# Optimization experiments

Hardware: AMD Instinct MI355X
Metric: run time of the kernel (lower is better)

Reference implementation:

```python
import jax, jax.numpy as jnp
import numpy as np

B, T, D, H, C = 256, 512, 300, 128, 6

def setup_inputs() -> dict:
    key = jax.random.key(0)
    ks = jax.random.split(key, 8)
    s = 1.0 / np.sqrt(H)  # PyTorch LSTM/Linear uniform init scale
    x = jax.random.normal(ks[0], (B, T, D), dtype=jnp.float32)
    lengths = jax.random.randint(ks[1], (B,), 1, T + 1)
    W_ih = jax.random.uniform(ks[2], (4 * H, D), minval=-s, maxval=s, dtype=jnp.float32)
    W_hh = jax.random.uniform(ks[3], (4 * H, H), minval=-s, maxval=s, dtype=jnp.float32)
    b_ih = jax.random.uniform(ks[4], (4 * H,), minval=-s, maxval=s, dtype=jnp.float32)
    b_hh = jax.random.uniform(ks[5], (4 * H,), minval=-s, maxval=s, dtype=jnp.float32)
    fc_w = jax.random.uniform(ks[6], (C, H), minval=-s, maxval=s, dtype=jnp.float32)
    fc_b = jax.random.uniform(ks[7], (C,), minval=-s, maxval=s, dtype=jnp.float32)
    return {"x": x, "W_ih": W_ih, "W_hh": W_hh, "b_ih": b_ih, "b_hh": b_hh,
            "fc_w": fc_w, "fc_b": fc_b, "lengths": lengths}

def _lstm_last_hidden(x, W_ih, W_hh, b_ih, b_hh, lengths):
    # Equivalent to pack_padded_sequence + nn.LSTM: the returned hidden[-1]
    # is the state at t = length-1 for each sequence. We run a masked scan:
    # state updates are frozen once t >= length.
    Bv, Tv, _ = x.shape
    Hv = W_hh.shape[1]
    xs = jnp.swapaxes(x, 0, 1)                              # [T, B, D]
    gx = jnp.einsum('tbd,gd->tbg', xs, W_ih) + b_ih + b_hh  # [T, B, 4H]
    mask = (jnp.arange(Tv)[:, None] < lengths[None, :])     # [T, B]

    def step(carry, inp):
        h, c = carry
        g, m = inp
        gates = g + h @ W_hh.T                              # [B, 4H]
        i, f, gg, o = jnp.split(gates, 4, axis=-1)          # PyTorch gate order i,f,g,o
        i = jax.nn.sigmoid(i)
        f = jax.nn.sigmoid(f)
        gg = jnp.tanh(gg)
        o = jax.nn.sigmoid(o)
        c_new = f * c + i * gg
        h_new = o * jnp.tanh(c_new)
        m = m[:, None]
        h = jnp.where(m, h_new, h)
        c = jnp.where(m, c_new, c)
        return (h, c), None

    h0 = jnp.zeros((Bv, Hv), dtype=x.dtype)
    c0 = jnp.zeros((Bv, Hv), dtype=x.dtype)
    (h, c), _ = jax.lax.scan(step, (h0, c0), (gx, mask))
    return h

def reference(x, W_ih, W_hh, b_ih, b_hh, fc_w, fc_b, lengths):
    h = _lstm_last_hidden(x, W_ih, W_hh, b_ih, b_hh, lengths)  # [B, H]
    return h @ fc_w.T + fc_b                                   # [B, 6]
```

## Files before the change

### kernel.cpp

```cpp
#include <hip/hip_runtime.h>
#include <hip/hip_bf16.h>
#include <stdint.h>
#include <type_traits>

#define NB 256
#define NT 512
#define ND 300
#define NH 128
#define NG 512
#define NC 6

typedef __attribute__((ext_vector_type(8))) short short8;
typedef __attribute__((ext_vector_type(4))) float f32x4;

static __device__ __forceinline__ float bf2f(unsigned int u) {
  return __builtin_bit_cast(float, (u & 0xffffu) << 16);
}
static __device__ __forceinline__ unsigned short f2bf(float f) {
  return __builtin_bit_cast(unsigned short, __float2bfloat16(f));
}
static __device__ __forceinline__ unsigned int packbf(float a, float b) {
  return (unsigned int)f2bf(a) | ((unsigned int)f2bf(b) << 16);
}
static __device__ __forceinline__ float ld1(const unsigned short* p) { return bf2f(*p); }
static __device__ __forceinline__ float ld1(const float* p) { return *p; }
static __device__ __forceinline__ void st1(unsigned short* p, float v) { *p = f2bf(v); }
static __device__ __forceinline__ void st1(float* p, float v) { *p = v; }

static __device__ __forceinline__ float sigmoid_fast(float x) {
  return __builtin_amdgcn_rcpf(1.f + __expf(-x));
}
static __device__ __forceinline__ float tanh_fast(float x) {
  return 1.f - 2.f * __builtin_amdgcn_rcpf(__expf(2.f * x) + 1.f);
}

static __device__ __forceinline__ uint2 load4bf_fast(const unsigned short* row, int k) {
  return *(const uint2*)(row + k);
}
static __device__ __forceinline__ uint2 load4bf_fast(const float* row, int k) {
  float4 f = *(const float4*)(row + k);
  uint2 v;
  v.x = packbf(f.x, f.y);
  v.y = packbf(f.z, f.w);
  return v;
}
static __device__ __forceinline__ uint2 load4bf(const unsigned short* row, int k, int lim) {
  if (k + 3 < lim) return load4bf_fast(row, k);
  unsigned int e0 = (k + 0 < lim) ? row[k + 0] : 0;
  unsigned int e1 = (k + 1 < lim) ? row[k + 1] : 0;
  unsigned int e2 = (k + 2 < lim) ? row[k + 2] : 0;
  unsigned int e3 = (k + 3 < lim) ? row[k + 3] : 0;
  uint2 v;
  v.x = e0 | (e1 << 16);
  v.y = e2 | (e3 << 16);
  return v;
}
static __device__ __forceinline__ uint2 load4bf(const float* row, int k, int lim) {
  if (k + 3 < lim) return load4bf_fast(row, k);
  float f0 = (k + 0 < lim) ? row[k + 0] : 0.f;
  float f1 = (k + 1 < lim) ? row[k + 1] : 0.f;
  float f2 = (k + 2 < lim) ? row[k + 2] : 0.f;
  float f3 = (k + 3 < lim) ? row[k + 3] : 0.f;
  uint2 v;
  v.x = packbf(f0, f1);
  v.y = packbf(f2, f3);
  return v;
}

__global__ void detect_dtype(const unsigned short* __restrict__ X, int* __restrict__ flag) {
  __shared__ int cnt;
  if (threadIdx.x == 0) cnt = 0;
  __syncthreads();
  int c = 0;
  for (int i = threadIdx.x; i < 512; i += 64) {
    unsigned int u = X[i];
    unsigned int e = (u >> 7) & 0xffu;
    if (u == 0u || (e >= 97u && e <= 157u)) c++;
  }
  atomicAdd(&cnt, c);
  __syncthreads();
  if (threadIdx.x == 0) *flag = (cnt >= 448) ? 0 : 1;
}

template <typename XT, typename GXT>
__global__ __launch_bounds__(256) void gx_gemm(const int* __restrict__ flag, int want,
                                               const XT* __restrict__ X,
                                               const XT* __restrict__ Wih,
                                               const XT* __restrict__ bih,
                                               const XT* __restrict__ bhh,
                                               const int* __restrict__ lengths,
                                               GXT* __restrict__ gx,
                                               int b_base, int t_base, int Tc) {
  if (*flag != want) return;
  const int mb = blockIdx.x;
  const int m0 = mb << 7;
  const int bc = m0 / Tc;
  const int trel0 = m0 % Tc;
  const int b = b_base + bc;
  const int t0 = t_base + trel0;
  const int len = lengths[b];
  if (t0 >= len) return;

  __shared__ unsigned short As[128][40];
  __shared__ unsigned short Bs[64][40];

  const int tid = threadIdx.x;
  const int lane = tid & 63;
  const int wave = tid >> 6;
  const int wm = wave & 1;
  const int wn = wave >> 1;
  const int lq = lane >> 4;
  const int lr = lane & 15;

  const int rA = tid >> 1, cA = (tid & 1) * 16;
  const int rB = tid >> 2, cB = (tid & 3) * 8;
  const XT* xrow = X + ((size_t)b * NT + t0 + rA) * ND;

  for (int nt = 0; nt < 8; ++nt) {
    const int n0 = nt << 6;
    const XT* wrow = Wih + (size_t)(n0 + rB) * ND;

    f32x4 acc[4][2];
#pragma unroll
    for (int i = 0; i < 4; ++i)
#pragma unroll
      for (int j = 0; j < 2; ++j) {
        f32x4 z = {0.f, 0.f, 0.f, 0.f};
        acc[i][j] = z;
      }

    uint2 av[2][4], bv[2][2];
#pragma unroll
    for (int g4 = 0; g4 < 4; ++g4) {
      av[0][g4] = load4bf_fast(xrow, cA + g4 * 4);
      av[1][g4] = load4bf_fast(xrow, 32 + cA + g4 * 4);
    }
#pragma unroll
    for (int g4 = 0; g4 < 2; ++g4) {
      bv[0][g4] = load4bf_fast(wrow, cB + g4 * 4);
      bv[1][g4] = load4bf_fast(wrow, 32 + cB + g4 * 4);
    }

#pragma unroll
    for (int kc9 = 0; kc9 < 10; ++kc9) {
      const int bi = kc9 & 1;
      __syncthreads();
#pragma unroll
      for (int g4 = 0; g4 < 4; ++g4) *(uint2*)&As[rA][cA + g4 * 4] = av[bi][g4];
#pragma unroll
      for (int g4 = 0; g4 < 2; ++g4) *(uint2*)&Bs[rB][cB + g4 * 4] = bv[bi][g4];
      __syncthreads();

      if (kc9 < 8) {
        const int kn = (kc9 + 2) * 32;
        if (kc9 < 7) {
#pragma unroll
          for (int g4 = 0; g4 < 4; ++g4) av[bi][g4] = load4bf_fast(xrow, kn + cA + g4 * 4);
#pragma unroll
          for (int g4 = 0; g4 < 2; ++g4) bv[bi][g4] = load4bf_fast(wrow, kn + cB + g4 * 4);
        } else {
#pragma unroll
          for (int g4 = 0; g4 < 4; ++g4) av[bi][g4] = load4bf(xrow, kn + cA + g4 * 4, ND);
#pragma unroll
          for (int g4 = 0; g4 < 2; ++g4) bv[bi][g4] = load4bf(wrow, kn + cB + g4 * 4, ND);
        }
      }

      short8 af[4], bq[2];
#pragma unroll
      for (int tm = 0; tm < 4; ++tm)
        af[tm] = *(const short8*)&As[wm * 64 + tm * 16 + lr][lq * 8];
#pragma unroll
      for (int tn = 0; tn < 2; ++tn)
        bq[tn] = *(const short8*)&Bs[wn * 32 + tn * 16 + lr][lq * 8];
#pragma unroll
      for (int tm = 0; tm < 4; ++tm)
#pragma unroll
        for (int tn = 0; tn < 2; ++tn)
          acc[tm][tn] =
              __builtin_amdgcn_mfma_f32_16x16x32_bf16(af[tm], bq[tn], acc[tm][tn], 0, 0, 0);
    }

    float bias_c[2];
#pragma unroll
    for (int tn = 0; tn < 2; ++tn) {
      const int col = n0 + wn * 32 + tn * 16 + lr;
      bias_c[tn] = ld1(bih + col) + ld1(bhh + col);
    }
#pragma unroll
    for (int tm = 0; tm < 4; ++tm)
#pragma unroll
      for (int tn = 0; tn < 2; ++tn)
#pragma unroll
        for (int rg = 0; rg < 4; ++rg) {
          const int tileRow = wm * 64 + tm * 16 + lq * 4 + rg;
          if (t0 + tileRow < len) {
            const int col = n0 + wn * 32 + tn * 16 + lr;
            st1(gx + (size_t)(m0 + tileRow) * NG + col, acc[tm][tn][rg] + bias_c[tn]);
          }
        }
  }
}

template <typename XT, typename GXT>
__global__ __launch_bounds__(512)
__attribute__((amdgpu_waves_per_eu(2, 2)))
void lstm_rec(const int* __restrict__ flag, int want,
              const GXT* __restrict__ gx,
              const XT* __restrict__ Whh,
              const XT* __restrict__ fcw,
              const XT* __restrict__ fcb,
              const int* __restrict__ lengths,
              XT* __restrict__ out,
              float* __restrict__ hstate,
              float* __restrict__ cstate,
              int b_base, int t_base, int Tc) {
  if (*flag != want) return;
  const int bc = blockIdx.x;
  const int b = b_base + bc;
  int len = lengths[b];
  if (len > NT) len = NT;
  if (len < 0) len = 0;
  const bool first = (t_base == 0);
  const bool last = (t_base + Tc >= NT);
  const int tend = (len < t_base + Tc) ? len : (t_base + Tc);
  if (!last && tend <= t_base) return;
  int nsteps = tend - t_base;
  if (nsteps < 0) nsteps = 0;

  const int tid = threadIdx.x;
  const int w8 = tid >> 6;
  const int l = tid & 63;
  const int q = l >> 4;
  const int m = l & 15;
  const int u0 = w8 * 16 + q * 4;
  const int r = m & 3;
  const int u = u0 + r;

  __shared__ __align__(16) unsigned short hpk[2][NH];
  __shared__ __align__(16) float hf[NH];

  short8 afr[4][4];
#pragma unroll
  for (int g = 0; g < 4; ++g) {
    const int row = g * NH + w8 * 16 + m;
    if constexpr (std::is_same_v<XT, unsigned short>) {
#pragma unroll
      for (int c = 0; c < 4; ++c)
        afr[g][c] = *(const short8*)(Whh + (size_t)row * NH + c * 32 + q * 8);
    } else {
#pragma unroll
      for (int c = 0; c < 4; ++c) {
        const float* p = Whh + (size_t)row * NH + c * 32 + q * 8;
        float4 f0 = *(const float4*)p;
        float4 f1 = *(const float4*)(p + 4);
        union { unsigned int uu[4]; short8 s; } cv2;
        cv2.uu[0] = packbf(f0.x, f0.y);
        cv2.uu[1] = packbf(f0.z, f0.w);
        cv2.uu[2] = packbf(f1.x, f1.y);
        cv2.uu[3] = packbf(f1.z, f1.w);
        afr[g][c] = cv2.s;
      }
    }
  }

  float hcur = 0.f, ccur = 0.f;
  if (!first) {
    hcur = hstate[(size_t)bc * NH + u];
    ccur = cstate[(size_t)bc * NH + u];
  }
  if (m < 4) hpk[0][u] = f2bf(hcur);
  __syncthreads();

  const GXT* gp = gx + (size_t)bc * Tc * NG + u;
  const int lastidx = (nsteps > 0) ? nsteps - 1 : 0;
  float g_c[4], g_n[4];
#pragma unroll
  for (int g = 0; g < 4; ++g) {
    g_c[g] = ld1(gp + g * NH);
    g_n[g] = ld1(gp + (size_t)((1 < lastidx) ? 1 : lastidx) * NG + g * NH);
  }

  for (int s = 0; s < nsteps; ++s) {
    int idx = s + 2;
    if (idx > lastidx) idx = lastidx;
    float g_f[4];
#pragma unroll
    for (int g = 0; g < 4; ++g) g_f[g] = ld1(gp + (size_t)idx * NG + g * NH);

    short8 bfr[4];
    const unsigned short* hrow = hpk[s & 1];
#pragma unroll
    for (int c = 0; c < 4; ++c) bfr[c] = *(const short8*)&hrow[c * 32 + q * 8];

    f32x4 acc[4];
#pragma unroll
    for (int g = 0; g < 4; ++g) {
      f32x4 z = {0.f, 0.f, 0.f, 0.f};
      acc[g] = z;
#pragma unroll
      for (int c = 0; c < 4; ++c)
        acc[g] = __builtin_amdgcn_mfma_f32_16x16x32_bf16(afr[g][c], bfr[c], acc[g], 0, 0, 0);
    }

    float pre[4];
#pragma unroll
    for (int g = 0; g < 4; ++g) {
      const float t0v = (r & 1) ? acc[g][1] : acc[g][0];
      const float t1v = (r & 1) ? acc[g][3] : acc[g][2];
      pre[g] = ((r & 2) ? t1v : t0v) + g_c[g];
    }
    const float ig = sigmoid_fast(pre[0]);
    const float fg = sigmoid_fast(pre[1]);
    const float gg = tanh_fast(pre[2]);
    const float og = sigmoid_fast(pre[3]);
    ccur = fmaf(fg, ccur, ig * gg);
    hcur = og * tanh_fast(ccur);
    if (m < 4) hpk[(s + 1) & 1][u] = f2bf(hcur);
    __syncthreads();

#pragma unroll
    for (int g = 0; g < 4; ++g) {
      g_c[g] = g_n[g];
      g_n[g] = g_f[g];
    }
  }

  if (!last) {
    if (m < 4) {
      hstate[(size_t)bc * NH + u] = hcur;
      cstate[(size_t)bc * NH + u] = ccur;
    }
  } else {
    if (m < 4) hf[u] = hcur;
    __syncthreads();
    if (tid < NC) {
      float acc = ld1(fcb + tid);
      const XT* wv = fcw + (size_t)tid * NH;
#pragma unroll
      for (int k = 0; k < NH; ++k) acc = fmaf(ld1(wv + k), hf[k], acc);
      st1(out + (size_t)b * NC + tid, acc);
    }
  }
}

template <typename XT, typename GXT>
static void run_variant(int want, const int* flag, void* const* d_in, XT* out,
                        GXT* gx, float* hstate, float* cstate, int NBc, int Tc,
                        hipStream_t stream) {
  const XT* X = (const XT*)d_in[0];
  const XT* Wih = (const XT*)d_in[1];
  const XT* Whh = (const XT*)d_in[2];
  const XT* bih = (const XT*)d_in[3];
  const XT* bhh = (const XT*)d_in[4];
  const XT* fcw = (const XT*)d_in[5];
  const XT* fcb = (const XT*)d_in[6];
  const int* lengths = (const int*)d_in[7];
  for (int bb = 0; bb < NB; bb += NBc) {
    for (int tb = 0; tb < NT; tb += Tc) {
      gx_gemm<XT, GXT><<<dim3((NBc * Tc) / 128), dim3(256), 0, stream>>>(
          flag, want, X, Wih, bih, bhh, lengths, gx, bb, tb, Tc);
      lstm_rec<XT, GXT><<<dim3(NBc), dim3(512), 0, stream>>>(
          flag, want, gx, Whh, fcw, fcb, lengths, out, hstate, cstate, bb, tb, Tc);
    }
  }
}

extern "C" void kernel_launch(void* const* d_in, const int* in_sizes, int n_in,
                              void* d_out, int out_size, void* d_ws, size_t ws_size,
                              hipStream_t stream) {
  int* flag = (int*)d_ws;
  detect_dtype<<<dim3(1), dim3(64), 0, stream>>>((const unsigned short*)d_in[0], flag);

  const size_t full_f32 = (size_t)NB * NT * NG * sizeof(float);
  const size_t full_bf16 = (size_t)NB * NT * NG * 2;
  const size_t base = 512;

  int NBc, Tc;
  char* gx_raw;
  float* hstate = (float*)((char*)d_ws + base);
  bool gx_is_f32;

  if (ws_size >= base + full_f32) {
    NBc = NB; Tc = NT; gx_is_f32 = true;
    gx_raw = (char*)d_ws + base;
  } else if (ws_size >= base + full_bf16) {
    NBc = NB; Tc = NT; gx_is_f32 = false;
    gx_raw = (char*)d_ws + base;
  } else {
    Tc = 128; gx_is_f32 = false;
    NBc = 1;
    for (int cand : {64, 16, 4}) {
      size_t need = base + (size_t)cand * NH * 2 * sizeof(float) + (size_t)cand * Tc * NG * 2;
      if (ws_size >= need) { NBc = cand; break; }
    }
    gx_raw = (char*)d_ws + base + (size_t)NBc * NH * 2 * sizeof(float);
  }
  float* cstate = hstate + (size_t)NBc * NH;

  if (gx_is_f32) {
    run_variant<unsigned short, float>(0, flag, d_in, (unsigned short*)d_out,
                                       (float*)gx_raw, hstate, cstate, NBc, Tc, stream);
    run_variant<float, float>(1, flag, d_in, (float*)d_out, (float*)gx_raw, hstate,
                              cstate, NBc, Tc, stream);
  } else {
    run_variant<unsigned short, unsigned short>(0, flag, d_in, (unsigned short*)d_out,
                                                (unsigned short*)gx_raw, hstate, cstate,
                                                NBc, Tc, stream);
    run_variant<float, unsigned short>(1, flag, d_in, (float*)d_out,
                                       (unsigned short*)gx_raw, hstate, cstate, NBc, Tc,
                                       stream);
  }
}
```

Measured before the change: 633.6 us.

## Stage full-K X tile in LDS once and retile gx GEMM to 64x128

```diff
diff --git a/kernel.cpp b/kernel.cpp
--- a/kernel.cpp
+++ b/kernel.cpp
@@ -93,7 +93,7 @@
                                                int b_base, int t_base, int Tc) {
   if (*flag != want) return;
   const int mb = blockIdx.x;
-  const int m0 = mb << 7;
+  const int m0 = mb << 6;
   const int bc = m0 / Tc;
   const int trel0 = m0 % Tc;
   const int b = b_base + bc;
@@ -101,8 +101,8 @@
   const int len = lengths[b];
   if (t0 >= len) return;
 
-  __shared__ unsigned short As[128][40];
-  __shared__ unsigned short Bs[64][40];
+  __shared__ unsigned short As[10][64][40];
+  __shared__ unsigned short Bs[2][128][40];
 
   const int tid = threadIdx.x;
   const int lane = tid & 63;
@@ -112,91 +112,103 @@
   const int lq = lane >> 4;
   const int lr = lane & 15;
 
-  const int rA = tid >> 1, cA = (tid & 1) * 16;
-  const int rB = tid >> 2, cB = (tid & 3) * 8;
+  const int rA = tid >> 2;
+  const int cA = (tid & 3) << 2;
   const XT* xrow = X + ((size_t)b * NT + t0 + rA) * ND;
-
-  for (int nt = 0; nt < 8; ++nt) {
-    const int n0 = nt << 6;
+  {
+    uint2 a0[10], a1[10];
+#pragma unroll
+    for (int kc = 0; kc < 9; ++kc) {
+      a0[kc] = load4bf_fast(xrow, kc * 32 + cA);
+      a1[kc] = load4bf_fast(xrow, kc * 32 + 16 + cA);
+    }
+    a0[9] = load4bf(xrow, 288 + cA, ND);
+    a1[9] = load4bf(xrow, 288 + 16 + cA, ND);
+#pragma unroll
+    for (int kc = 0; kc < 10; ++kc) {
+      *(uint2*)&As[kc][rA][cA] = a0[kc];
+      *(uint2*)&As[kc][rA][16 + cA] = a1[kc];
+    }
+  }
+
+  const int rB = tid >> 1;
+  const int cB = (tid & 1) << 2;
+
+  for (int nt = 0; nt < 4; ++nt) {
+    const int n0 = nt << 7;
     const XT* wrow = Wih + (size_t)(n0 + rB) * ND;
 
-    f32x4 acc[4][2];
-#pragma unroll
-    for (int i = 0; i < 4; ++i)
-#pragma unroll
-      for (int j = 0; j < 2; ++j) {
+    f32x4 acc[2][4];
+#pragma unroll
+    for (int i = 0; i < 2; ++i)
+#pragma unroll
+      for (int j = 0; j < 4; ++j) {
         f32x4 z = {0.f, 0.f, 0.f, 0.f};
         acc[i][j] = z;
       }
 
-    uint2 av[2][4], bv[2][2];
-#pragma unroll
-    for (int g4 = 0; g4 < 4; ++g4) {
-      av[0][g4] = load4bf_fast(xrow, cA + g4 * 4);
-      av[1][g4] = load4bf_fast(xrow, 32 + cA + g4 * 4);
-    }
-#pragma unroll
-    for (int g4 = 0; g4 < 2; ++g4) {
-      bv[0][g4] = load4bf_fast(wrow, cB + g4 * 4);
-      bv[1][g4] = load4bf_fast(wrow, 32 + cB + g4 * 4);
-    }
-
-#pragma unroll
-    for (int kc9 = 0; kc9 < 10; ++kc9) {
-      const int bi = kc9 & 1;
-      __syncthreads();
-#pragma unroll
-      for (int g4 = 0; g4 < 4; ++g4) *(uint2*)&As[rA][cA + g4 * 4] = av[bi][g4];
-#pragma unroll
-      for (int g4 = 0; g4 < 2; ++g4) *(uint2*)&Bs[rB][cB + g4 * 4] = bv[bi][g4];
-      __syncthreads();
-
-      if (kc9 < 8) {
-        const int kn = (kc9 + 2) * 32;
-        if (kc9 < 7) {
-#pragma unroll
-          for (int g4 = 0; g4 < 4; ++g4) av[bi][g4] = load4bf_fast(xrow, kn + cA + g4 * 4);
-#pragma unroll
-          for (int g4 = 0; g4 < 2; ++g4) bv[bi][g4] = load4bf_fast(wrow, kn + cB + g4 * 4);
+    uint2 bv[2][4];
+#pragma unroll
+    for (int g4 = 0; g4 < 4; ++g4) bv[0][g4] = load4bf_fast(wrow, cB + g4 * 8);
+#pragma unroll
+    for (int g4 = 0; g4 < 4; ++g4) bv[1][g4] = load4bf_fast(wrow, 32 + cB + g4 * 8);
+
+    __syncthreads();
+#pragma unroll
+    for (int g4 = 0; g4 < 4; ++g4) *(uint2*)&Bs[0][rB][cB + g4 * 8] = bv[0][g4];
+    __syncthreads();
+
+#pragma unroll
+    for (int kc = 0; kc < 10; ++kc) {
+      const int bi = kc & 1;
+      if (kc < 9) {
+#pragma unroll
+        for (int g4 = 0; g4 < 4; ++g4)
+          *(uint2*)&Bs[bi ^ 1][rB][cB + g4 * 8] = bv[bi ^ 1][g4];
+      }
+      if (kc < 8) {
+        const int kn = (kc + 2) * 32;
+        if (kc < 7) {
+#pragma unroll
+          for (int g4 = 0; g4 < 4; ++g4) bv[bi][g4] = load4bf_fast(wrow, kn + cB + g4 * 8);
         } else {
 #pragma unroll
-          for (int g4 = 0; g4 < 4; ++g4) av[bi][g4] = load4bf(xrow, kn + cA + g4 * 4, ND);
-#pragma unroll
-          for (int g4 = 0; g4 < 2; ++g4) bv[bi][g4] = load4bf(wrow, kn + cB + g4 * 4, ND);
+          for (int g4 = 0; g4 < 4; ++g4) bv[bi][g4] = load4bf(wrow, kn + cB + g4 * 8, ND);
         }
       }
 
-      short8 af[4], bq[2];
-#pragma unroll
-      for (int tm = 0; tm < 4; ++tm)
-        af[tm] = *(const short8*)&As[wm * 64 + tm * 16 + lr][lq * 8];
-#pragma unroll
-      for (int tn = 0; tn < 2; ++tn)
-        bq[tn] = *(const short8*)&Bs[wn * 32 + tn * 16 + lr][lq * 8];
-#pragma unroll
-      for (int tm = 0; tm < 4; ++tm)
-#pragma unroll
-        for (int tn = 0; tn < 2; ++tn)
+      short8 af[2], bq[4];
+#pragma unroll
+      for (int tm = 0; tm < 2; ++tm)
+        af[tm] = *(const short8*)&As[kc][wm * 32 + tm * 16 + lr][lq * 8];
+#pragma unroll
+      for (int tn = 0; tn < 4; ++tn)
+        bq[tn] = *(const short8*)&Bs[bi][wn * 64 + tn * 16 + lr][lq * 8];
+#pragma unroll
+      for (int tm = 0; tm < 2; ++tm)
+#pragma unroll
+        for (int tn = 0; tn < 4; ++tn)
           acc[tm][tn] =
               __builtin_amdgcn_mfma_f32_16x16x32_bf16(af[tm], bq[tn], acc[tm][tn], 0, 0, 0);
-    }
-
-    float bias_c[2];
-#pragma unroll
-    for (int tn = 0; tn < 2; ++tn) {
-      const int col = n0 + wn * 32 + tn * 16 + lr;
+      __syncthreads();
+    }
+
+    float bias_c[4];
+#pragma unroll
+    for (int tn = 0; tn < 4; ++tn) {
+      const int col = n0 + wn * 64 + tn * 16 + lr;
       bias_c[tn] = ld1(bih + col) + ld1(bhh + col);
     }
 #pragma unroll
-    for (int tm = 0; tm < 4; ++tm)
-#pragma unroll
-      for (int tn = 0; tn < 2; ++tn)
+    for (int tm = 0; tm < 2; ++tm)
+#pragma unroll
+      for (int tn = 0; tn < 4; ++tn)
 #pragma unroll
         for (int rg = 0; rg < 4; ++rg) {
-          const int tileRow = wm * 64 + tm * 16 + lq * 4 + rg;
-          if (t0 + tileRow < len) {
-            const int col = n0 + wn * 32 + tn * 16 + lr;
-            st1(gx + (size_t)(m0 + tileRow) * NG + col, acc[tm][tn][rg] + bias_c[tn]);
+          const int row = wm * 32 + tm * 16 + lq * 4 + rg;
+          if (t0 + row < len) {
+            const int col = n0 + wn * 64 + tn * 16 + lr;
+            st1(gx + (size_t)(m0 + row) * NG + col, acc[tm][tn][rg] + bias_c[tn]);
           }
         }
   }
@@ -358,7 +370,7 @@
   const int* lengths = (const int*)d_in[7];
   for (int bb = 0; bb < NB; bb += NBc) {
     for (int tb = 0; tb < NT; tb += Tc) {
-      gx_gemm<XT, GXT><<<dim3((NBc * Tc) / 128), dim3(256), 0, stream>>>(
+      gx_gemm<XT, GXT><<<dim3((NBc * Tc) / 64), dim3(256), 0, stream>>>(
           flag, want, X, Wih, bih, bhh, lengths, gx, bb, tb, Tc);
       lstm_rec<XT, GXT><<<dim3(NBc), dim3(512), 0, stream>>>(
           flag, want, gx, Whh, fcw, fcb, lengths, out, hstate, cstate, bb, tb, Tc);
```

After: 617.2 us. 2.6% less time.

## Fuse input-projection GEMM into recurrent LSTM kernel with windowed overlap

Applied to the files above, without the earlier changes.

```diff
diff --git a/kernel.cpp b/kernel.cpp
--- a/kernel.cpp
+++ b/kernel.cpp
@@ -33,6 +33,8 @@
 static __device__ __forceinline__ float tanh_fast(float x) {
   return 1.f - 2.f * __builtin_amdgcn_rcpf(__expf(2.f * x) + 1.f);
 }
+
+#define BARRIER_LGKM() asm volatile("s_waitcnt lgkmcnt(0)\n\ts_barrier" ::: "memory")
 
 static __device__ __forceinline__ uint2 load4bf_fast(const unsigned short* row, int k) {
   return *(const uint2*)(row + k);
@@ -82,163 +84,105 @@
   if (threadIdx.x == 0) *flag = (cnt >= 448) ? 0 : 1;
 }
 
-template <typename XT, typename GXT>
-__global__ __launch_bounds__(256) void gx_gemm(const int* __restrict__ flag, int want,
-                                               const XT* __restrict__ X,
-                                               const XT* __restrict__ Wih,
-                                               const XT* __restrict__ bih,
-                                               const XT* __restrict__ bhh,
-                                               const int* __restrict__ lengths,
-                                               GXT* __restrict__ gx,
-                                               int b_base, int t_base, int Tc) {
+template <typename XT>
+__global__ __launch_bounds__(256) void wprep(const int* __restrict__ flag, int want,
+                                             const XT* __restrict__ Wih,
+                                             unsigned short* __restrict__ Wpre) {
   if (*flag != want) return;
-  const int mb = blockIdx.x;
-  const int m0 = mb << 7;
-  const int bc = m0 / Tc;
-  const int trel0 = m0 % Tc;
-  const int b = b_base + bc;
-  const int t0 = t_base + trel0;
-  const int len = lengths[b];
-  if (t0 >= len) return;
-
-  __shared__ unsigned short As[128][40];
-  __shared__ unsigned short Bs[64][40];
-
-  const int tid = threadIdx.x;
-  const int lane = tid & 63;
-  const int wave = tid >> 6;
-  const int wm = wave & 1;
-  const int wn = wave >> 1;
-  const int lq = lane >> 4;
-  const int lr = lane & 15;
-
-  const int rA = tid >> 1, cA = (tid & 1) * 16;
-  const int rB = tid >> 2, cB = (tid & 3) * 8;
-  const XT* xrow = X + ((size_t)b * NT + t0 + rA) * ND;
-
-  for (int nt = 0; nt < 8; ++nt) {
-    const int n0 = nt << 6;
-    const XT* wrow = Wih + (size_t)(n0 + rB) * ND;
-
-    f32x4 acc[4][2];
-#pragma unroll
-    for (int i = 0; i < 4; ++i)
-#pragma unroll
-      for (int j = 0; j < 2; ++j) {
-        f32x4 z = {0.f, 0.f, 0.f, 0.f};
-        acc[i][j] = z;
-      }
-
-    uint2 av[2][4], bv[2][2];
-#pragma unroll
-    for (int g4 = 0; g4 < 4; ++g4) {
-      av[0][g4] = load4bf_fast(xrow, cA + g4 * 4);
-      av[1][g4] = load4bf_fast(xrow, 32 + cA + g4 * 4);
-    }
-#pragma unroll
-    for (int g4 = 0; g4 < 2; ++g4) {
-      bv[0][g4] = load4bf_fast(wrow, cB + g4 * 4);
-      bv[1][g4] = load4bf_fast(wrow, 32 + cB + g4 * 4);
-    }
-
-#pragma unroll
-    for (int kc9 = 0; kc9 < 10; ++kc9) {
-      const int bi = kc9 & 1;
-      __syncthreads();
-#pragma unroll
-      for (int g4 = 0; g4 < 4; ++g4) *(uint2*)&As[rA][cA + g4 * 4] = av[bi][g4];
-#pragma unroll
-      for (int g4 = 0; g4 < 2; ++g4) *(uint2*)&Bs[rB][cB + g4 * 4] = bv[bi][g4];
-      __syncthreads();
-
-      if (kc9 < 8) {
-        const int kn = (kc9 + 2) * 32;
-        if (kc9 < 7) {
-#pragma unroll
-          for (int g4 = 0; g4 < 4; ++g4) av[bi][g4] = load4bf_fast(xrow, kn + cA + g4 * 4);
-#pragma unroll
-          for (int g4 = 0; g4 < 2; ++g4) bv[bi][g4] = load4bf_fast(wrow, kn + cB + g4 * 4);
-        } else {
-#pragma unroll
-          for (int g4 = 0; g4 < 4; ++g4) av[bi][g4] = load4bf(xrow, kn + cA + g4 * 4, ND);
-#pragma unroll
-          for (int g4 = 0; g4 < 2; ++g4) bv[bi][g4] = load4bf(wrow, kn + cB + g4 * 4, ND);
-        }
-      }
-
-      short8 af[4], bq[2];
-#pragma unroll
-      for (int tm = 0; tm < 4; ++tm)
-        af[tm] = *(const short8*)&As[wm * 64 + tm * 16 + lr][lq * 8];
-#pragma unroll
-      for (int tn = 0; tn < 2; ++tn)
-        bq[tn] = *(const short8*)&Bs[wn * 32 + tn * 16 + lr][lq * 8];
-#pragma unroll
-      for (int tm = 0; tm < 4; ++tm)
-#pragma unroll
-        for (int tn = 0; tn < 2; ++tn)
-          acc[tm][tn] =
-              __builtin_amdgcn_mfma_f32_16x16x32_bf16(af[tm], bq[tn], acc[tm][tn], 0, 0, 0);
-    }
-
-    float bias_c[2];
-#pragma unroll
-    for (int tn = 0; tn < 2; ++tn) {
-      const int col = n0 + wn * 32 + tn * 16 + lr;
-      bias_c[tn] = ld1(bih + col) + ld1(bhh + col);
-    }
-#pragma unroll
-    for (int tm = 0; tm < 4; ++tm)
-#pragma unroll
-      for (int tn = 0; tn < 2; ++tn)
-#pragma unroll
-        for (int rg = 0; rg < 4; ++rg) {
-          const int tileRow = wm * 64 + tm * 16 + lq * 4 + rg;
-          if (t0 + tileRow < len) {
-            const int col = n0 + wn * 32 + tn * 16 + lr;
-            st1(gx + (size_t)(m0 + tileRow) * NG + col, acc[tm][tn][rg] + bias_c[tn]);
-          }
-        }
-  }
-}
-
-template <typename XT, typename GXT>
+  const int i = blockIdx.x * 256 + threadIdx.x;
+  const int rtg = i / 640;
+  const int rem = i % 640;
+  const int c = rem >> 6;
+  const int l2 = rem & 63;
+  const int row = rtg * 16 + (l2 & 15);
+  const int kb = c * 32 + (l2 >> 4) * 8;
+  union { unsigned short v[8]; short8 s; } o;
+#pragma unroll
+  for (int j = 0; j < 8; ++j) {
+    const int k = kb + j;
+    o.v[j] = (k < ND) ? f2bf(ld1(Wih + (size_t)row * ND + k)) : (unsigned short)0;
+  }
+  *(short8*)(Wpre + (size_t)i * 8) = o.s;
+}
+
+
+#define ISSUE_A(cc, ss)                                                         \
+  do {                                                                          \
+    if constexpr (WPRE) {                                                       \
+      _Pragma("unroll") for (int rt = 0; rt < 4; ++rt)                          \
+          sA##ss[rt] = *(const short8*)(Wpre +                                  \
+              (size_t)((((w8 << 2) + rt) * 10 + (cc)) * 64 + l) * 8);           \
+    } else {                                                                    \
+      _Pragma("unroll") for (int rt = 0; rt < 4; ++rt) {                        \
+        const XT* wr_ = Wih + (size_t)(w8 * 64 + rt * 16 + lr) * ND;            \
+        uA##ss[rt][0] = load4bf(wr_, (cc) * 32 + lq * 8, ND);                   \
+        uA##ss[rt][1] = load4bf(wr_, (cc) * 32 + lq * 8 + 4, ND);               \
+      }                                                                         \
+    }                                                                           \
+  } while (0)
+
+#define CONSUME_A(cc, ss)                                                       \
+  do {                                                                          \
+    const short8 bfrG_ = *(const short8*)&xb1[lr][(cc) * 32 + lq * 8];          \
+    _Pragma("unroll") for (int rt = 0; rt < 4; ++rt) {                          \
+      short8 a_;                                                                \
+      if constexpr (WPRE) {                                                     \
+        a_ = sA##ss[rt];                                                        \
+      } else {                                                                  \
+        union { uint2 u2[2]; short8 s; } cv_;                                   \
+        cv_.u2[0] = uA##ss[rt][0];                                              \
+        cv_.u2[1] = uA##ss[rt][1];                                              \
+        a_ = cv_.s;                                                             \
+      }                                                                         \
+      accG[rt] = __builtin_amdgcn_mfma_f32_16x16x32_bf16(a_, bfrG_, accG[rt],   \
+                                                         0, 0, 0);              \
+    }                                                                           \
+  } while (0)
+
+#define WRITEBACK_RT(rt_)                                                       \
+  do {                                                                          \
+    f32x4 o_;                                                                   \
+    _Pragma("unroll") for (int rg = 0; rg < 4; ++rg)                            \
+        o_[rg] = accG[rt_][rg] + biasr[rt_][rg];                                \
+    *(f32x4*)&gb1[lr][w8 * 64 + (rt_) * 16 + lq * 4] = o_;                      \
+  } while (0)
+
+template <typename XT, bool WPRE>
 __global__ __launch_bounds__(512)
 __attribute__((amdgpu_waves_per_eu(2, 2)))
-void lstm_rec(const int* __restrict__ flag, int want,
-              const GXT* __restrict__ gx,
-              const XT* __restrict__ Whh,
-              const XT* __restrict__ fcw,
-              const XT* __restrict__ fcb,
-              const int* __restrict__ lengths,
-              XT* __restrict__ out,
-              float* __restrict__ hstate,
-              float* __restrict__ cstate,
-              int b_base, int t_base, int Tc) {
+void lstm_fused(const int* __restrict__ flag, int want,
+                const XT* __restrict__ X,
+                const XT* __restrict__ Wih,
+                const XT* __restrict__ Whh,
+                const XT* __restrict__ bih,
+                const XT* __restrict__ bhh,
+                const XT* __restrict__ fcw,
+                const XT* __restrict__ fcb,
+                const int* __restrict__ lengths,
+                XT* __restrict__ out,
+                const unsigned short* __restrict__ Wpre) {
   if (*flag != want) return;
-  const int bc = blockIdx.x;
-  const int b = b_base + bc;
+  const int b = blockIdx.x;
   int len = lengths[b];
   if (len > NT) len = NT;
   if (len < 0) len = 0;
-  const bool first = (t_base == 0);
-  const bool last = (t_base + Tc >= NT);
-  const int tend = (len < t_base + Tc) ? len : (t_base + Tc);
-  if (!last && tend <= t_base) return;
-  int nsteps = tend - t_base;
-  if (nsteps < 0) nsteps = 0;
+  const int nwin = (len + 15) >> 4;
+
+  __shared__ __align__(16) float gw[2][16][520];
+  __shared__ __align__(16) unsigned short xw[2][16][328];
+  __shared__ __align__(16) unsigned short hpk[2][NH];
+  __shared__ __align__(16) float hf[NH];
 
   const int tid = threadIdx.x;
   const int w8 = tid >> 6;
   const int l = tid & 63;
   const int q = l >> 4;
   const int m = l & 15;
+  const int lq = q;
+  const int lr = m;
   const int u0 = w8 * 16 + q * 4;
   const int r = m & 3;
   const int u = u0 + r;
-
-  __shared__ __align__(16) unsigned short hpk[2][NH];
-  __shared__ __align__(16) float hf[NH];
 
   short8 afr[4][4];
 #pragma unroll
@@ -264,107 +208,192 @@
     }
   }
 
+  float biasr[4][4];
+#pragma unroll
+  for (int rt = 0; rt < 4; ++rt)
+#pragma unroll
+    for (int rg = 0; rg < 4; ++rg) {
+      const int g = w8 * 64 + rt * 16 + lq * 4 + rg;
+      biasr[rt][rg] = ld1(bih + g) + ld1(bhh + g);
+    }
+
+  if (tid < 448) {
+    const int bi = tid / 224;
+    const int rr = (tid % 224) / 14;
+    const int cc = 300 + (tid % 14) * 2;
+    *(unsigned int*)&xw[bi][rr][cc] = 0u;
+  }
+
+  if (nwin > 0) {
+#pragma unroll
+    for (int ii = 0; ii < 3; ++ii) {
+      const int j = tid + ii * 512;
+      if (j < 1200) {
+        const int row = j / 75, col = (j % 75) * 4;
+        const XT* src = X + ((size_t)b * NT + row) * ND + col;
+        *(uint2*)&xw[0][row][col] = load4bf_fast(src, 0);
+      }
+    }
+  }
+  __syncthreads();
+
+  short8 sA0[4], sA1[4];
+  uint2 uA0[4][2], uA1[4][2];
+  f32x4 accG[4];
+  unsigned short (*xb1)[328] = xw[0];
+  float (*gb1)[520] = gw[0];
+
+  if (nwin > 0) {
+#pragma unroll
+    for (int rt = 0; rt < 4; ++rt) { f32x4 z = {0.f, 0.f, 0.f, 0.f}; accG[rt] = z; }
+    ISSUE_A(0, 0);
+    ISSUE_A(1, 1); CONSUME_A(0, 0);
+    ISSUE_A(2, 0); CONSUME_A(1, 1);
+    ISSUE_A(3, 1); CONSUME_A(2, 0);
+    ISSUE_A(4, 0); CONSUME_A(3, 1);
+    ISSUE_A(5, 1); CONSUME_A(4, 0);
+    ISSUE_A(6, 0); CONSUME_A(5, 1);
+    ISSUE_A(7, 1); CONSUME_A(6, 0);
+    ISSUE_A(8, 0); CONSUME_A(7, 1);
+    ISSUE_A(9, 1); CONSUME_A(8, 0);
+    CONSUME_A(9, 1);
+    WRITEBACK_RT(0); WRITEBACK_RT(1); WRITEBACK_RT(2); WRITEBACK_RT(3);
+  }
+
+  if (nwin > 1) {
+#pragma unroll
+    for (int ii = 0; ii < 3; ++ii) {
+      const int j = tid + ii * 512;
+      if (j < 1200) {
+        const int row = j / 75, col = (j % 75) * 4;
+        const XT* src = X + ((size_t)b * NT + 16 + row) * ND + col;
+        *(uint2*)&xw[1][row][col] = load4bf_fast(src, 0);
+      }
+    }
+  }
+
   float hcur = 0.f, ccur = 0.f;
-  if (!first) {
-    hcur = hstate[(size_t)bc * NH + u];
-    ccur = cstate[(size_t)bc * NH + u];
-  }
-  if (m < 4) hpk[0][u] = f2bf(hcur);
+  if (m < 4) hpk[0][u] = f2bf(0.f);
   __syncthreads();
 
-  const GXT* gp = gx + (size_t)bc * Tc * NG + u;
-  const int lastidx = (nsteps > 0) ? nsteps - 1 : 0;
-  float g_c[4], g_n[4];
-#pragma unroll
-  for (int g = 0; g < 4; ++g) {
-    g_c[g] = ld1(gp + g * NH);
-    g_n[g] = ld1(gp + (size_t)((1 < lastidx) ? 1 : lastidx) * NG + g * NH);
-  }
-
-  for (int s = 0; s < nsteps; ++s) {
-    int idx = s + 2;
-    if (idx > lastidx) idx = lastidx;
-    float g_f[4];
-#pragma unroll
-    for (int g = 0; g < 4; ++g) g_f[g] = ld1(gp + (size_t)idx * NG + g * NH);
-
-    short8 bfr[4];
-    const unsigned short* hrow = hpk[s & 1];
-#pragma unroll
-    for (int c = 0; c < 4; ++c) bfr[c] = *(const short8*)&hrow[c * 32 + q * 8];
-
-    f32x4 acc[4];
-#pragma unroll
-    for (int g = 0; g < 4; ++g) {
-      f32x4 z = {0.f, 0.f, 0.f, 0.f};
-      acc[g] = z;
-#pragma unroll
-      for (int c = 0; c < 4; ++c)
-        acc[g] = __builtin_amdgcn_mfma_f32_16x16x32_bf16(afr[g][c], bfr[c], acc[g], 0, 0, 0);
-    }
-
-    float pre[4];
-#pragma unroll
-    for (int g = 0; g < 4; ++g) {
-      const float t0v = (r & 1) ? acc[g][1] : acc[g][0];
-      const float t1v = (r & 1) ? acc[g][3] : acc[g][2];
-      pre[g] = ((r & 2) ? t1v : t0v) + g_c[g];
-    }
-    const float ig = sigmoid_fast(pre[0]);
-    const float fg = sigmoid_fast(pre[1]);
-    const float gg = tanh_fast(pre[2]);
-    const float og = sigmoid_fast(pre[3]);
-    ccur = fmaf(fg, ccur, ig * gg);
-    hcur = og * tanh_fast(ccur);
-    if (m < 4) hpk[(s + 1) & 1][u] = f2bf(hcur);
-    __syncthreads();
-
-#pragma unroll
-    for (int g = 0; g < 4; ++g) {
-      g_c[g] = g_n[g];
-      g_n[g] = g_f[g];
-    }
-  }
-
-  if (!last) {
-    if (m < 4) {
-      hstate[(size_t)bc * NH + u] = hcur;
-      cstate[(size_t)bc * NH + u] = ccur;
-    }
-  } else {
-    if (m < 4) hf[u] = hcur;
-    __syncthreads();
-    if (tid < NC) {
-      float acc = ld1(fcb + tid);
-      const XT* wv = fcw + (size_t)tid * NH;
-#pragma unroll
-      for (int k = 0; k < NH; ++k) acc = fmaf(ld1(wv + k), hf[k], acc);
-      st1(out + (size_t)b * NC + tid, acc);
-    }
-  }
-}
-
-template <typename XT, typename GXT>
-static void run_variant(int want, const int* flag, void* const* d_in, XT* out,
-                        GXT* gx, float* hstate, float* cstate, int NBc, int Tc,
-                        hipStream_t stream) {
-  const XT* X = (const XT*)d_in[0];
-  const XT* Wih = (const XT*)d_in[1];
-  const XT* Whh = (const XT*)d_in[2];
-  const XT* bih = (const XT*)d_in[3];
-  const XT* bhh = (const XT*)d_in[4];
-  const XT* fcw = (const XT*)d_in[5];
-  const XT* fcb = (const XT*)d_in[6];
-  const int* lengths = (const int*)d_in[7];
-  for (int bb = 0; bb < NB; bb += NBc) {
-    for (int tb = 0; tb < NT; tb += Tc) {
-      gx_gemm<XT, GXT><<<dim3((NBc * Tc) / 128), dim3(256), 0, stream>>>(
-          flag, want, X, Wih, bih, bhh, lengths, gx, bb, tb, Tc);
-      lstm_rec<XT, GXT><<<dim3(NBc), dim3(512), 0, stream>>>(
-          flag, want, gx, Whh, fcw, fcb, lengths, out, hstate, cstate, bb, tb, Tc);
-    }
-  }
-}
+  for (int w = 0; w < nwin; ++w) {
+    const int rem = len - w * 16;
+    const int tlim = (rem < 16) ? rem : 16;
+    const bool gemm_on = (w + 1 < nwin);
+    const bool stage_on = (w + 2 < nwin);
+    float (*gb0)[520] = gw[w & 1];
+    xb1 = xw[(w + 1) & 1];
+    gb1 = gw[(w + 1) & 1];
+    if (gemm_on) {
+#pragma unroll
+      for (int rt = 0; rt < 4; ++rt) { f32x4 z = {0.f, 0.f, 0.f, 0.f}; accG[rt] = z; }
+    }
+    float4 rf[3];
+    uint2 ru[3];
+
+#pragma unroll 4
+    for (int st = 0; st < 16; ++st) {
+      if (st >= tlim) break;
+
+      float g_c[4];
+#pragma unroll
+      for (int g = 0; g < 4; ++g) g_c[g] = gb0[st][g * 128 + u];
+      short8 bfr[4];
+      const unsigned short* hrow = hpk[st & 1];
+#pragma unroll
+      for (int c = 0; c < 4; ++c) bfr[c] = *(const short8*)&hrow[c * 32 + q * 8];
+      f32x4 acc[4];
+#pragma unroll
+      for (int g = 0; g < 4; ++g) {
+        f32x4 z = {0.f, 0.f, 0.f, 0.f};
+        acc[g] = z;
+#pragma unroll
+        for (int c = 0; c < 4; ++c)
+          acc[g] = __builtin_amdgcn_mfma_f32_16x16x32_bf16(afr[g][c], bfr[c], acc[g], 0, 0, 0);
+      }
+      float pre[4];
+#pragma unroll
+      for (int g = 0; g < 4; ++g) {
+        const float t0v = (r & 1) ? acc[g][1] : acc[g][0];
+        const float t1v = (r & 1) ? acc[g][3] : acc[g][2];
+        pre[g] = ((r & 2) ? t1v : t0v) + g_c[g];
+      }
+      const float ig = sigmoid_fast(pre[0]);
+      const float fg = sigmoid_fast(pre[1]);
+      const float gg = tanh_fast(pre[2]);
+      const float og = sigmoid_fast(pre[3]);
+      ccur = fmaf(fg, ccur, ig * gg);
+      hcur = og * tanh_fast(ccur);
+      if (m < 4) hpk[(st + 1) & 1][u] = f2bf(hcur);
+
+      if (gemm_on) {
+        if (st == 0) { ISSUE_A(0, 0); }
+        if (st == 1) { ISSUE_A(1, 1); CONSUME_A(0, 0); }
+        if (st == 2) { ISSUE_A(2, 0); CONSUME_A(1, 1); }
+        if (st == 3) { ISSUE_A(3, 1); CONSUME_A(2, 0); }
+        if (st == 4) { ISSUE_A(4, 0); CONSUME_A(3, 1); }
+        if (st == 5) { ISSUE_A(5, 1); CONSUME_A(4, 0); }
+        if (st == 6) { ISSUE_A(6, 0); CONSUME_A(5, 1); }
+        if (st == 7) { ISSUE_A(7, 1); CONSUME_A(6, 0); }
+        if (st == 8) { ISSUE_A(8, 0); CONSUME_A(7, 1); }
+        if (st == 9) { ISSUE_A(9, 1); CONSUME_A(8, 0); }
+        if (st == 10) { CONSUME_A(9, 1); }
+        if (st == 11) { WRITEBACK_RT(0); }
+        if (st == 12) { WRITEBACK_RT(1); }
+        if (st == 13) { WRITEBACK_RT(2); }
+        if (st == 14) { WRITEBACK_RT(3); }
+      }
+
+      if (stage_on) {
+        if (st == 0) {
+#pragma unroll
+          for (int ii = 0; ii < 3; ++ii) {
+            const int j = tid + ii * 512;
+            if (j < 1200) {
+              const int row = j / 75, col = (j % 75) * 4;
+              const XT* src = X + ((size_t)b * NT + (w + 2) * 16 + row) * ND + col;
+              if constexpr (std::is_same_v<XT, float>) rf[ii] = *(const float4*)src;
+              else ru[ii] = *(const uint2*)src;
+            }
+          }
+        }
+        if (st == 8) {
+#pragma unroll
+          for (int ii = 0; ii < 3; ++ii) {
+            const int j = tid + ii * 512;
+            if (j < 1200) {
+              const int row = j / 75, col = (j % 75) * 4;
+              uint2 v;
+              if constexpr (std::is_same_v<XT, float>) {
+                v.x = packbf(rf[ii].x, rf[ii].y);
+                v.y = packbf(rf[ii].z, rf[ii].w);
+              } else {
+                v = ru[ii];
+              }
+              *(uint2*)&xw[w & 1][row][col] = v;
+            }
+          }
+        }
+      }
+
+      BARRIER_LGKM();
+    }
+  }
+
+  if (m < 4) hf[u] = hcur;
+  __syncthreads();
+  if (tid < NC) {
+    float acc = ld1(fcb + tid);
+    const XT* wv = fcw + (size_t)tid * NH;
+#pragma unroll
+    for (int k = 0; k < NH; ++k) acc = fmaf(ld1(wv + k), hf[k], acc);
+    st1(out + (size_t)b * NC + tid, acc);
+  }
+}
+
+#undef ISSUE_A
+#undef CONSUME_A
+#undef WRITEBACK_RT
 
 extern "C" void kernel_launch(void* const* d_in, const int* in_sizes, int n_in,
                               void* d_out, int out_size, void* d_ws, size_t ws_size,
@@ -372,43 +401,36 @@
   int* flag = (int*)d_ws;
   detect_dtype<<<dim3(1), dim3(64), 0, stream>>>((const unsigned short*)d_in[0], flag);
 
-  const size_t full_f32 = (size_t)NB * NT * NG * sizeof(float);
-  const size_t full_bf16 = (size_t)NB * NT * NG * 2;
-  const size_t base = 512;
-
-  int NBc, Tc;
-  char* gx_raw;
-  float* hstate = (float*)((char*)d_ws + base);
-  bool gx_is_f32;
-
-  if (ws_size >= base + full_f32) {
-    NBc = NB; Tc = NT; gx_is_f32 = true;
-    gx_raw = (char*)d_ws + base;
-  } else if (ws_size >= base + full_bf16) {
-    NBc = NB; Tc = NT; gx_is_f32 = false;
-    gx_raw = (char*)d_ws + base;
+  unsigned short* wsW = (unsigned short*)((char*)d_ws + 512);
+  const size_t wpre_bytes = (size_t)32 * 10 * 64 * 8 * 2;
+  const bool use_pre = ws_size >= 512 + wpre_bytes;
+
+  const unsigned short* Xu = (const unsigned short*)d_in[0];
+  const float* Xf = (const float*)d_in[0];
+
+  if (use_pre) {
+    wprep<unsigned short><<<dim3(80), dim3(256), 0, stream>>>(
+        flag, 0, (const unsigned short*)d_in[1], wsW);
+    wprep<float><<<dim3(80), dim3(256), 0, stream>>>(
+        flag, 1, (const float*)d_in[1], wsW);
+    lstm_fused<unsigned short, true><<<dim3(NB), dim3(512), 0, stream>>>(
+        flag, 0, Xu, (const unsigned short*)d_in[1], (const unsigned short*)d_in[2],
+        (const unsigned short*)d_in[3], (const unsigned short*)d_in[4],
+        (const unsigned short*)d_in[5], (const unsigned short*)d_in[6],
+        (const int*)d_in[7], (unsigned short*)d_out, wsW);
+    lstm_fused<float, true><<<dim3(NB), dim3(512), 0, stream>>>(
+        flag, 1, Xf, (const float*)d_in[1], (const float*)d_in[2],
+        (const float*)d_in[3], (const float*)d_in[4], (const float*)d_in[5],
+        (const float*)d_in[6], (const int*)d_in[7], (float*)d_out, wsW);
   } else {
-    Tc = 128; gx_is_f32 = false;
-    NBc = 1;
-    for (int cand : {64, 16, 4}) {
-      size_t need = base + (size_t)cand * NH * 2 * sizeof(float) + (size_t)cand * Tc * NG * 2;
-      if (ws_size >= need) { NBc = cand; break; }
-    }
-    gx_raw = (char*)d_ws + base + (size_t)NBc * NH * 2 * sizeof(float);
-  }
-  float* cstate = hstate + (size_t)NBc * NH;
-
-  if (gx_is_f32) {
-    run_variant<unsigned short, float>(0, flag, d_in, (unsigned short*)d_out,
-                                       (float*)gx_raw, hstate, cstate, NBc, Tc, stream);
-    run_variant<float, float>(1, flag, d_in, (float*)d_out, (float*)gx_raw, hstate,
-                              cstate, NBc, Tc, stream);
-  } else {
-    run_variant<unsigned short, unsigned short>(0, flag, d_in, (unsigned short*)d_out,
-                                                (unsigned short*)gx_raw, hstate, cstate,
-                                                NBc, Tc, stream);
-    run_variant<float, unsigned short>(1, flag, d_in, (float*)d_out,
-                                       (unsigned short*)gx_raw, hstate, cstate, NBc, Tc,
-                                       stream);
-  }
-}
+    lstm_fused<unsigned short, false><<<dim3(NB), dim3(512), 0, stream>>>(
+        flag, 0, Xu, (const unsigned short*)d_in[1], (const unsigned short*)d_in[2],
+        (const unsigned short*)d_in[3], (const unsigned short*)d_in[4],
+        (const unsigned short*)d_in[5], (const unsigned short*)d_in[6],
+        (const int*)d_in[7], (unsigned short*)d_out, nullptr);
+    lstm_fused<float, false><<<dim3(NB), dim3(512), 0, stream>>>(
+        flag, 1, Xf, (const float*)d_in[1], (const float*)d_in[2],
+        (const float*)d_in[3], (const float*)d_in[4], (const float*)d_in[5],
+        (const float*)d_in[6], (const int*)d_in[7], (float*)d_out, nullptr);
+  }
+}
```

Measured after the change: 774.3 us. 1.22x slower.
